# Kernel optimization log

Hardware: AMD Instinct MI355X
Metric: run time of the kernel (lower is better)

Reference implementation:

```python
import jax, jax.numpy as jnp
import numpy as np

TOP_K = 8
N_EXPERTS = 64
ALPHA = 0.1
NORM_TOPK = True
SEQ_AUX = True


def setup_inputs() -> dict:
    key = jax.random.key(0)
    k1, k2 = jax.random.split(key)
    B, S, H = 4, 4096, 2048
    hidden_states = jax.random.normal(k1, (B, S, H), dtype=jnp.float32)
    # kaiming_uniform_(a=sqrt(5)) => bound = 1/sqrt(fan_in)
    bound = 1.0 / np.sqrt(H)
    weight = jax.random.uniform(k2, (N_EXPERTS, H), dtype=jnp.float32,
                                minval=-bound, maxval=bound)
    return {"hidden_states": hidden_states, "weight": weight}


def reference(hidden_states, weight):
    B, S, H = hidden_states.shape
    E, K = N_EXPERTS, TOP_K
    x = hidden_states.reshape(-1, H)                 # [T, H], T = B*S
    logits = jnp.einsum('th,eh->te', x, weight)      # gating GEMM
    scores = jax.nn.softmax(logits, axis=-1)         # [T, E]
    topk_weight, topk_idx = jax.lax.top_k(scores, K) # [T, K]
    if K > 1 and NORM_TOPK:
        topk_weight = topk_weight / (topk_weight.sum(-1, keepdims=True) + 1e-20)

    # batch-level load stats (bincount over selections)
    expert_loads = jnp.zeros((E,), jnp.float32).at[topk_idx.reshape(-1)].add(1.0)

    # sequence-level auxiliary load-balancing loss
    if SEQ_AUX:
        idx_b = topk_idx.reshape(B, S * K)           # [B, S*K]
        ce = jnp.zeros((B, E), jnp.float32)
        ce = ce.at[jnp.arange(B)[:, None], idx_b].add(1.0)
        ce = ce / (S * K / E)
        mean_scores = scores.reshape(B, S, E).mean(axis=1)   # [B, E]
        aux_loss = (ce * mean_scores).sum(axis=1).mean() * ALPHA
    else:
        ce = jax.nn.one_hot(topk_idx.reshape(-1), E).mean(0)
        Pi = scores.mean(0)
        aux_loss = (Pi * ce * E).sum() * ALPHA

    return (topk_idx, topk_weight, aux_loss, expert_loads)
```

## Files before the change

### kernel.cpp

```cpp
#include <hip/hip_runtime.h>
#include <hip/hip_bf16.h>
#include <math.h>

#define TOK 16384
#define HDIM 2048
#define NE 64
#define NB 4
#define KTOP 8
#define KC 64
#define NC (HDIM / KC)
#define BT 32

typedef __attribute__((ext_vector_type(8))) __bf16 bf16x8;
typedef __attribute__((ext_vector_type(4))) float f32x4;
typedef unsigned int uint;

__device__ __forceinline__ uint asu(float f) { union { float f; uint u; } c; c.f = f; return c.u; }
__device__ __forceinline__ float asf(uint u) { union { uint u; float f; } c; c.u = u; return c.f; }

__device__ __forceinline__ void split3(float v, uint& h, uint& m, uint& l) {
  uint u = asu(v);
  h = u & 0xffff0000u;
  float d = v - asf(h);
  m = asu(d) & 0xffff0000u;
  float d2 = d - asf(m);
  l = asu(d2);
}

__device__ __forceinline__ void split8(float4 a, float4 b,
                                       bf16x8& h8, bf16x8& m8, bf16x8& l8) {
  union { uint4 u; bf16x8 v; } H, M, L;
  uint h0, m0, l0, h1, m1, l1;
  split3(a.x, h0, m0, l0); split3(a.y, h1, m1, l1);
  H.u.x = (h0 >> 16) | (h1 & 0xffff0000u);
  M.u.x = (m0 >> 16) | (m1 & 0xffff0000u);
  L.u.x = (l0 >> 16) | (l1 & 0xffff0000u);
  split3(a.z, h0, m0, l0); split3(a.w, h1, m1, l1);
  H.u.y = (h0 >> 16) | (h1 & 0xffff0000u);
  M.u.y = (m0 >> 16) | (m1 & 0xffff0000u);
  L.u.y = (l0 >> 16) | (l1 & 0xffff0000u);
  split3(b.x, h0, m0, l0); split3(b.y, h1, m1, l1);
  H.u.z = (h0 >> 16) | (h1 & 0xffff0000u);
  M.u.z = (m0 >> 16) | (m1 & 0xffff0000u);
  L.u.z = (l0 >> 16) | (l1 & 0xffff0000u);
  split3(b.z, h0, m0, l0); split3(b.w, h1, m1, l1);
  H.u.w = (h0 >> 16) | (h1 & 0xffff0000u);
  M.u.w = (m0 >> 16) | (m1 & 0xffff0000u);
  L.u.w = (l0 >> 16) | (l1 & 0xffff0000u);
  h8 = H.v; m8 = M.v; l8 = L.v;
}

__device__ __forceinline__ void gl_lds16(const void* g, void* l) {
  __builtin_amdgcn_global_load_lds(
      (const __attribute__((address_space(1))) void*)g,
      (__attribute__((address_space(3))) void*)l, 16, 0, 0);
}

__global__ __launch_bounds__(256) void wsplit(const float* __restrict__ w,
                                              char* __restrict__ wpk,
                                              float* __restrict__ stats) {
  if (blockIdx.x == 0 && threadIdx.x < 128) {
    *(float4*)(stats + threadIdx.x * 4) = make_float4(0.f, 0.f, 0.f, 0.f);
  }
  int t = blockIdx.x * 256 + threadIdx.x;
  int lane = t & 63;
  int f2 = (t >> 6) & 1, half = (t >> 7) & 1, ks = (t >> 8) & 1, c = t >> 9;
  int e = half * 32 + f2 * 16 + (lane & 15);
  int k = c * 64 + ks * 32 + ((lane >> 4) << 3);
  const float* p = w + (size_t)e * HDIM + k;
  bf16x8 h8, m8, l8;
  split8(*(const float4*)p, *(const float4*)(p + 4), h8, m8, l8);
  union { bf16x8 v; uint4 u; } H, M, L;
  H.v = h8; M.v = m8; L.v = l8;
  size_t base = (size_t)c * 24576 + (size_t)ks * 12288 + (size_t)half * 6144
              + (size_t)f2 * 3072 + (size_t)lane * 16;
  *(uint4*)(wpk + base) = H.u;
  *(uint4*)(wpk + base + 1024) = M.u;
  *(uint4*)(wpk + base + 2048) = L.u;
}

__global__ __launch_bounds__(256, 2) void gate_fused(const float* __restrict__ x,
                                                     const char* __restrict__ wpk,
                                                     float* __restrict__ out,
                                                     float* __restrict__ ce,
                                                     float* __restrict__ ssum) {
  __shared__ __align__(16) char lds[49152];
  __shared__ float hist[NE];

  const int tid = threadIdx.x;
  const int bid = blockIdx.x;
  const int t0 = bid * BT;
  const int b = bid >> 7;
  const int lane = tid & 63;
  const int wid = tid >> 6;
  const int half = wid & 1;
  const int tg = (wid >> 1) << 4;

  if (tid < NE) hist[tid] = 0.f;

  char* buf0 = lds;
  char* buf1 = lds + 24576;

  const float* xrow = x + (size_t)(t0 + tg + (lane & 15)) * HDIM + ((lane >> 4) << 3);

  f32x4 acc[2] = {{0.f, 0.f, 0.f, 0.f}, {0.f, 0.f, 0.f, 0.f}};

  {
    const char* wsp0 = wpk + (size_t)lane * 16;
#pragma unroll
    for (int i = 0; i < 6; ++i)
      gl_lds16(wsp0 + (i * 4 + wid) * 1024, buf0 + (i * 4 + wid) * 1024);
  }
  float4 xa0 = *(const float4*)(xrow);
  float4 xa1 = *(const float4*)(xrow + 4);
  float4 xa2 = *(const float4*)(xrow + 32);
  float4 xa3 = *(const float4*)(xrow + 36);
  float4 xb0 = *(const float4*)(xrow + 64);
  float4 xb1 = *(const float4*)(xrow + 68);
  float4 xb2 = *(const float4*)(xrow + 96);
  float4 xb3 = *(const float4*)(xrow + 100);
  asm volatile("s_waitcnt vmcnt(8)" ::: "memory");
  __builtin_amdgcn_s_barrier();
  asm volatile("" ::: "memory");

#define CHUNK(c, X0, X1, X2, X3, BR, BW)                                        \
  {                                                                             \
    if ((c) + 1 < NC) {          \
      const char* wsp = wpk + (size_t)((c) + 1) * 24576 + (size_t)lane * 16;    \
      _Pragma("unroll")                                                         \
      for (int i = 0; i < 6; ++i)                                               \
        gl_lds16(wsp + (i * 4 + wid) * 1024, BW + (i * 4 + wid) * 1024);        \
    }                                                                           \
    bf16x8 ah0, am0, al0, ah1, am1, al1;                     \
    split8(X0, X1, ah0, am0, al0);                                              \
    split8(X2, X3, ah1, am1, al1);                                              \
    if ((c) + 2 < NC) {                                    \
      const float* xp = xrow + (size_t)((c) + 2) * 64;                          \
      X0 = *(const float4*)(xp);                                                \
      X1 = *(const float4*)(xp + 4);                                            \
      X2 = *(const float4*)(xp + 32);                                           \
      X3 = *(const float4*)(xp + 36);                                           \
    }                                                                           \
    _Pragma("unroll")                                 \
    for (int f2 = 0; f2 < 2; ++f2) {                                            \
      const char* bb0 = BR + half * 6144 + f2 * 3072 + lane * 16;               \
      bf16x8 bh = *(const bf16x8*)(bb0);                                        \
      bf16x8 bm = *(const bf16x8*)(bb0 + 1024);                                 \
      bf16x8 bl = *(const bf16x8*)(bb0 + 2048);                                 \
      acc[f2] = __builtin_amdgcn_mfma_f32_16x16x32_bf16(ah0, bh, acc[f2], 0, 0, 0); \
      acc[f2] = __builtin_amdgcn_mfma_f32_16x16x32_bf16(ah0, bm, acc[f2], 0, 0, 0); \
      acc[f2] = __builtin_amdgcn_mfma_f32_16x16x32_bf16(am0, bh, acc[f2], 0, 0, 0); \
      acc[f2] = __builtin_amdgcn_mfma_f32_16x16x32_bf16(ah0, bl, acc[f2], 0, 0, 0); \
      acc[f2] = __builtin_amdgcn_mfma_f32_16x16x32_bf16(al0, bh, acc[f2], 0, 0, 0); \
      acc[f2] = __builtin_amdgcn_mfma_f32_16x16x32_bf16(am0, bm, acc[f2], 0, 0, 0); \
      const char* bb1 = BR + 12288 + half * 6144 + f2 * 3072 + lane * 16;       \
      bf16x8 kh = *(const bf16x8*)(bb1);                                        \
      bf16x8 km = *(const bf16x8*)(bb1 + 1024);                                 \
      bf16x8 kl = *(const bf16x8*)(bb1 + 2048);                                 \
      acc[f2] = __builtin_amdgcn_mfma_f32_16x16x32_bf16(ah1, kh, acc[f2], 0, 0, 0); \
      acc[f2] = __builtin_amdgcn_mfma_f32_16x16x32_bf16(ah1, km, acc[f2], 0, 0, 0); \
      acc[f2] = __builtin_amdgcn_mfma_f32_16x16x32_bf16(am1, kh, acc[f2], 0, 0, 0); \
      acc[f2] = __builtin_amdgcn_mfma_f32_16x16x32_bf16(ah1, kl, acc[f2], 0, 0, 0); \
      acc[f2] = __builtin_amdgcn_mfma_f32_16x16x32_bf16(al1, kh, acc[f2], 0, 0, 0); \
      acc[f2] = __builtin_amdgcn_mfma_f32_16x16x32_bf16(am1, km, acc[f2], 0, 0, 0); \
    }                                                                           \
          \
    if ((c) < NC - 2) { asm volatile("s_waitcnt vmcnt(4)" ::: "memory"); }      \
    else              { asm volatile("s_waitcnt vmcnt(0)" ::: "memory"); }      \
    __builtin_amdgcn_s_barrier();                                               \
    asm volatile("" ::: "memory");                                              \
  }

#pragma unroll 1
  for (int cc = 0; cc < NC; cc += 2) {
    CHUNK(cc,     xa0, xa1, xa2, xa3, buf0, buf1);
    CHUNK(cc + 1, xb0, xb1, xb2, xb3, buf1, buf0);
  }
#undef CHUNK

  float (*sc)[33] = (float(*)[33])lds;
#pragma unroll
  for (int f2 = 0; f2 < 2; ++f2) {
    int e = half * 32 + f2 * 16 + (lane & 15);
    int tk = tg + ((lane >> 4) << 2);
    sc[e][tk + 0] = acc[f2][0];
    sc[e][tk + 1] = acc[f2][1];
    sc[e][tk + 2] = acc[f2][2];
    sc[e][tk + 3] = acc[f2][3];
  }
  __syncthreads();

  const int t = tid >> 3;
  const int j = tid & 7;
  float p[8];
#pragma unroll
  for (int i = 0; i < 8; ++i) p[i] = sc[j * 8 + i][t];

  float m = p[0];
#pragma unroll
  for (int i = 1; i < 8; ++i) m = fmaxf(m, p[i]);
  m = fmaxf(m, __shfl_xor(m, 1, 8));
  m = fmaxf(m, __shfl_xor(m, 2, 8));
  m = fmaxf(m, __shfl_xor(m, 4, 8));
  float s = 0.f;
#pragma unroll
  for (int i = 0; i < 8; ++i) { p[i] = __expf(p[i] - m); s += p[i]; }
  s += __shfl_xor(s, 1, 8);
  s += __shfl_xor(s, 2, 8);
  s += __shfl_xor(s, 4, 8);
  float inv = 1.f / s;
#pragma unroll
  for (int i = 0; i < 8; ++i) { p[i] *= inv; sc[j * 8 + i][t] = p[i]; }

  unsigned used = 0;
  float wsum = 0.f;
  float wv[KTOP];
  int wi_[KTOP];
#pragma unroll
  for (int sel = 0; sel < KTOP; ++sel) {
    float bv = -1.f;
    int bi = 0;
#pragma unroll
    for (int i = 0; i < 8; ++i) {
      bool ok = !((used >> i) & 1u);
      if (ok && p[i] > bv) { bv = p[i]; bi = i; }
    }
    int ge = j * 8 + bi;
#pragma unroll
    for (int mk = 1; mk < 8; mk <<= 1) {
      float ov = __shfl_xor(bv, mk, 8);
      int og = __shfl_xor(ge, mk, 8);
      if (ov > bv || (ov == bv && og < ge)) { bv = ov; ge = og; }
    }
    if ((ge >> 3) == j) used |= 1u << (ge & 7);
    wv[sel] = bv;
    wi_[sel] = ge;
    wsum += bv;
  }
  if (j == 0) {
    float winv = 1.f / (wsum + 1e-20f);
#pragma unroll
    for (int sel = 0; sel < KTOP; ++sel) {
      out[(size_t)(t0 + t) * KTOP + sel] = (float)wi_[sel];
      out[(size_t)TOK * KTOP + (size_t)(t0 + t) * KTOP + sel] = wv[sel] * winv;
      atomicAdd(&hist[wi_[sel]], 1.f);
    }
  }
  __syncthreads();

  if (tid < NE) {
    float ssl = 0.f;
#pragma unroll
    for (int tt = 0; tt < BT; ++tt) ssl += sc[tid][tt];
    atomicAdd(&ssum[b * NE + tid], ssl);
    atomicAdd(&ce[b * NE + tid], hist[tid]);
  }
}

__global__ __launch_bounds__(64) void gate_final(const float* __restrict__ ce,
                                                 const float* __restrict__ ssum,
                                                 float* __restrict__ out) {
  const int e = threadIdx.x;
  float loads = 0.f, aux = 0.f;
#pragma unroll
  for (int b = 0; b < NB; ++b) {
    float c = ce[b * 64 + e];
    loads += c;
    aux += (c / 512.0f) * (ssum[b * 64 + e] / 4096.0f);
  }
  out[(size_t)2 * TOK * KTOP + 1 + e] = loads;
#pragma unroll
  for (int off = 32; off > 0; off >>= 1) aux += __shfl_down(aux, off);
  if (e == 0) out[(size_t)2 * TOK * KTOP] = aux * (0.1f / 4.0f);
}

extern "C" void kernel_launch(void* const* d_in, const int* in_sizes, int n_in,
                              void* d_out, int out_size, void* d_ws, size_t ws_size,
                              hipStream_t stream) {
  const float* x = (const float*)d_in[0];
  const float* w = (const float*)d_in[1];
  float* out = (float*)d_out;

  char* wpk = (char*)d_ws;
  float* ce = (float*)(wpk + (size_t)NC * 24576);
  float* ssum = ce + NB * NE;

  wsplit<<<dim3(64), dim3(256), 0, stream>>>(w, wpk, ce);
  gate_fused<<<dim3(TOK / BT), dim3(256), 0, stream>>>(x, wpk, out, ce, ssum);
  gate_final<<<dim3(1), dim3(64), 0, stream>>>(ce, ssum, out);
}
```

Before: 66.28 us.

## Stage activation tiles through LDS with direct global-to-LDS loads

Activation (x) tiles are no longer loaded into registers two chunks ahead. They are now staged into double-buffered LDS with the same global-to-LDS async loads used for the weights, and read back from LDS for splitting. This frees registers and unifies the pipeline. In exchange, LDS per block grows from 48KB to 64KB, each chunk adds LDS reads, and the wait becomes vmcnt(0) every chunk, which shortens the prefetch depth for x.

Result: faster. 59.00 us (median of 3 runs) (-11.0%).

```diff
diff --git a/kernel.cpp b/kernel.cpp
--- a/kernel.cpp
+++ b/kernel.cpp
@@ -84,7 +84,7 @@
                                                      float* __restrict__ out,
                                                      float* __restrict__ ce,
                                                      float* __restrict__ ssum) {
-  __shared__ __align__(16) char lds[49152];
+  __shared__ __align__(16) char lds[65536];
   __shared__ float hist[NE];
 
   const int tid = threadIdx.x;
@@ -94,95 +94,81 @@
   const int lane = tid & 63;
   const int wid = tid >> 6;
   const int half = wid & 1;
-  const int tg = (wid >> 1) << 4;
+  const int tg = (wid >> 1);
 
   if (tid < NE) hist[tid] = 0.f;
 
-  char* buf0 = lds;
-  char* buf1 = lds + 24576;
-
-  const float* xrow = x + (size_t)(t0 + tg + (lane & 15)) * HDIM + ((lane >> 4) << 3);
+  const char* xsg[2];
+  int xdo_[2];
+#pragma unroll
+  for (int r = 0; r < 2; ++r) {
+    int s = r * 256 + tid;
+    int stg = s >> 8, sks = (s >> 7) & 1, sq = (s >> 6) & 1, ln = s & 63;
+    xsg[r] = (const char*)(x + (size_t)(t0 + stg * 16 + (ln & 15)) * HDIM
+                           + sks * 32 + ((ln >> 4) << 3) + sq * 4);
+    xdo_[r] = (r * 256 + wid * 64) * 16;
+  }
+  const char* wsrc = wpk + (size_t)lane * 16;
 
   f32x4 acc[2] = {{0.f, 0.f, 0.f, 0.f}, {0.f, 0.f, 0.f, 0.f}};
 
-  {
-    const char* wsp0 = wpk + (size_t)lane * 16;
-#pragma unroll
-    for (int i = 0; i < 6; ++i)
-      gl_lds16(wsp0 + (i * 4 + wid) * 1024, buf0 + (i * 4 + wid) * 1024);
-  }
-  float4 xa0 = *(const float4*)(xrow);
-  float4 xa1 = *(const float4*)(xrow + 4);
-  float4 xa2 = *(const float4*)(xrow + 32);
-  float4 xa3 = *(const float4*)(xrow + 36);
-  float4 xb0 = *(const float4*)(xrow + 64);
-  float4 xb1 = *(const float4*)(xrow + 68);
-  float4 xb2 = *(const float4*)(xrow + 96);
-  float4 xb3 = *(const float4*)(xrow + 100);
-  asm volatile("s_waitcnt vmcnt(8)" ::: "memory");
+#define STAGE(cc, sel)                                                        \
+  {                                                                           \
+    char* wdst = lds + (sel) * 24576;                                         \
+    const char* wp_ = wsrc + (size_t)(cc) * 24576;                            \
+    _Pragma("unroll")                                                         \
+    for (int i = 0; i < 6; ++i)                                               \
+      gl_lds16(wp_ + (i * 4 + wid) * 1024, wdst + (i * 4 + wid) * 1024);      \
+    char* xdst = lds + 49152 + (sel) * 8192;                                  \
+    _Pragma("unroll")                                                         \
+    for (int r = 0; r < 2; ++r)                                               \
+      gl_lds16(xsg[r] + (size_t)(cc) * 256, xdst + xdo_[r]);                  \
+  }
+
+  STAGE(0, 0);
+  asm volatile("s_waitcnt vmcnt(0)" ::: "memory");
   __builtin_amdgcn_s_barrier();
   asm volatile("" ::: "memory");
 
-#define CHUNK(c, X0, X1, X2, X3, BR, BW)                                        \
-  {                                                                             \
-    if ((c) + 1 < NC) {          \
-      const char* wsp = wpk + (size_t)((c) + 1) * 24576 + (size_t)lane * 16;    \
-      _Pragma("unroll")                                                         \
-      for (int i = 0; i < 6; ++i)                                               \
-        gl_lds16(wsp + (i * 4 + wid) * 1024, BW + (i * 4 + wid) * 1024);        \
-    }                                                                           \
-    bf16x8 ah0, am0, al0, ah1, am1, al1;                     \
-    split8(X0, X1, ah0, am0, al0);                                              \
-    split8(X2, X3, ah1, am1, al1);                                              \
-    if ((c) + 2 < NC) {                                    \
-      const float* xp = xrow + (size_t)((c) + 2) * 64;                          \
-      X0 = *(const float4*)(xp);                                                \
-      X1 = *(const float4*)(xp + 4);                                            \
-      X2 = *(const float4*)(xp + 32);                                           \
-      X3 = *(const float4*)(xp + 36);                                           \
-    }                                                                           \
-    _Pragma("unroll")                                 \
-    for (int f2 = 0; f2 < 2; ++f2) {                                            \
-      const char* bb0 = BR + half * 6144 + f2 * 3072 + lane * 16;               \
-      bf16x8 bh = *(const bf16x8*)(bb0);                                        \
-      bf16x8 bm = *(const bf16x8*)(bb0 + 1024);                                 \
-      bf16x8 bl = *(const bf16x8*)(bb0 + 2048);                                 \
-      acc[f2] = __builtin_amdgcn_mfma_f32_16x16x32_bf16(ah0, bh, acc[f2], 0, 0, 0); \
-      acc[f2] = __builtin_amdgcn_mfma_f32_16x16x32_bf16(ah0, bm, acc[f2], 0, 0, 0); \
-      acc[f2] = __builtin_amdgcn_mfma_f32_16x16x32_bf16(am0, bh, acc[f2], 0, 0, 0); \
-      acc[f2] = __builtin_amdgcn_mfma_f32_16x16x32_bf16(ah0, bl, acc[f2], 0, 0, 0); \
-      acc[f2] = __builtin_amdgcn_mfma_f32_16x16x32_bf16(al0, bh, acc[f2], 0, 0, 0); \
-      acc[f2] = __builtin_amdgcn_mfma_f32_16x16x32_bf16(am0, bm, acc[f2], 0, 0, 0); \
-      const char* bb1 = BR + 12288 + half * 6144 + f2 * 3072 + lane * 16;       \
-      bf16x8 kh = *(const bf16x8*)(bb1);                                        \
-      bf16x8 km = *(const bf16x8*)(bb1 + 1024);                                 \
-      bf16x8 kl = *(const bf16x8*)(bb1 + 2048);                                 \
-      acc[f2] = __builtin_amdgcn_mfma_f32_16x16x32_bf16(ah1, kh, acc[f2], 0, 0, 0); \
-      acc[f2] = __builtin_amdgcn_mfma_f32_16x16x32_bf16(ah1, km, acc[f2], 0, 0, 0); \
-      acc[f2] = __builtin_amdgcn_mfma_f32_16x16x32_bf16(am1, kh, acc[f2], 0, 0, 0); \
-      acc[f2] = __builtin_amdgcn_mfma_f32_16x16x32_bf16(ah1, kl, acc[f2], 0, 0, 0); \
-      acc[f2] = __builtin_amdgcn_mfma_f32_16x16x32_bf16(al1, kh, acc[f2], 0, 0, 0); \
-      acc[f2] = __builtin_amdgcn_mfma_f32_16x16x32_bf16(am1, km, acc[f2], 0, 0, 0); \
-    }                                                                           \
-          \
-    if ((c) < NC - 2) { asm volatile("s_waitcnt vmcnt(4)" ::: "memory"); }      \
-    else              { asm volatile("s_waitcnt vmcnt(0)" ::: "memory"); }      \
-    __builtin_amdgcn_s_barrier();                                               \
-    asm volatile("" ::: "memory");                                              \
-  }
-
 #pragma unroll 1
-  for (int cc = 0; cc < NC; cc += 2) {
-    CHUNK(cc,     xa0, xa1, xa2, xa3, buf0, buf1);
-    CHUNK(cc + 1, xb0, xb1, xb2, xb3, buf1, buf0);
-  }
-#undef CHUNK
-
-  float (*sc)[33] = (float(*)[33])lds;
+  for (int c = 0; c < NC; ++c) {
+    const int sel = c & 1;
+    if (c + 1 < NC) STAGE(c + 1, sel ^ 1);
+
+    char* wb = lds + sel * 24576;
+    char* xb = lds + 49152 + sel * 8192 + tg * 4096;
+#pragma unroll
+    for (int ks = 0; ks < 2; ++ks) {
+      float4 X0 = *(const float4*)(xb + ks * 2048 + lane * 16);
+      float4 X1 = *(const float4*)(xb + ks * 2048 + 1024 + lane * 16);
+      bf16x8 ah, am, al;
+      split8(X0, X1, ah, am, al);
+      const char* wk = wb + ks * 12288 + half * 6144 + lane * 16;
+#pragma unroll
+      for (int f2 = 0; f2 < 2; ++f2) {
+        const char* bb = wk + f2 * 3072;
+        bf16x8 bh = *(const bf16x8*)(bb);
+        bf16x8 bm = *(const bf16x8*)(bb + 1024);
+        bf16x8 bl = *(const bf16x8*)(bb + 2048);
+        acc[f2] = __builtin_amdgcn_mfma_f32_16x16x32_bf16(ah, bh, acc[f2], 0, 0, 0);
+        acc[f2] = __builtin_amdgcn_mfma_f32_16x16x32_bf16(ah, bm, acc[f2], 0, 0, 0);
+        acc[f2] = __builtin_amdgcn_mfma_f32_16x16x32_bf16(am, bh, acc[f2], 0, 0, 0);
+        acc[f2] = __builtin_amdgcn_mfma_f32_16x16x32_bf16(ah, bl, acc[f2], 0, 0, 0);
+        acc[f2] = __builtin_amdgcn_mfma_f32_16x16x32_bf16(al, bh, acc[f2], 0, 0, 0);
+        acc[f2] = __builtin_amdgcn_mfma_f32_16x16x32_bf16(am, bm, acc[f2], 0, 0, 0);
+      }
+    }
+    asm volatile("s_waitcnt vmcnt(0)" ::: "memory");
+    __builtin_amdgcn_s_barrier();
+    asm volatile("" ::: "memory");
+  }
+#undef STAGE
+
+  float (*sc)[BT + 1] = (float(*)[BT + 1])lds;
 #pragma unroll
   for (int f2 = 0; f2 < 2; ++f2) {
     int e = half * 32 + f2 * 16 + (lane & 15);
-    int tk = tg + ((lane >> 4) << 2);
+    int tk = tg * 16 + ((lane >> 4) << 2);
     sc[e][tk + 0] = acc[f2][0];
     sc[e][tk + 1] = acc[f2][1];
     sc[e][tk + 2] = acc[f2][2];
```
